# Optimization experiments

Hardware: AMD Instinct MI355X
Metric: run time of the kernel (lower is better)

## Reference

```python
import jax, jax.numpy as jnp
import numpy as np

M_DIM = 128   # vec_dim m
L_BAS = 64    # bas_dim L
RANK = 8      # sliding window length
BATCH = 32
SEQ = 2048


def _make_bbasis(L, m):
    # Bbasis[k, i] = cos(2*pi*(k+1)/(i+2)), fixed buffer
    k = jnp.arange(L, dtype=jnp.float32)[:, None]
    i = jnp.arange(m, dtype=jnp.float32)[None, :]
    return jnp.cos(2.0 * jnp.pi * (k + 1.0) / (i + 2.0))


def setup_inputs() -> dict:
    key = jax.random.key(0)
    k1, k2 = jax.random.split(key)
    seq_batch = jax.random.normal(k1, (BATCH, SEQ, M_DIM), dtype=jnp.float32)
    M = jnp.eye(M_DIM, dtype=jnp.float32)                     # nn.init.eye_
    Acoeff = jax.random.uniform(k2, (M_DIM, L_BAS), dtype=jnp.float32,
                                minval=-0.1, maxval=0.1)      # uniform(-0.1, 0.1)
    Bbasis = _make_bbasis(L_BAS, M_DIM)
    return {"seq_batch": seq_batch, "M": M, "Acoeff": Acoeff, "Bbasis": Bbasis}


def reference(seq_batch, M, Acoeff, Bbasis):
    B, S, m = seq_batch.shape
    L = Acoeff.shape[1]
    Nw = S - RANK + 1  # number of sliding windows (linear mode, stride 1)

    # unfold-equivalent: gather contiguous windows [B, Nw, RANK, m]
    idx = jnp.arange(Nw)[:, None] + jnp.arange(RANK)[None, :]
    windows = seq_batch[:, idx, :]
    agg = windows.mean(axis=2)              # rank_op='avg' -> [B, Nw, m]
    agg = jnp.einsum('bwm,nm->bwn', agg, M)  # agg @ M.T (linear map)

    # position-indexed basis target: N(k)[i] = Acoeff[i, k%L] * Bbasis[k%L, i]
    kmod = jnp.arange(Nw) % L
    Nk = Acoeff.T[kmod] * Bbasis[kmod]       # [Nw, m]

    # mean squared deviation over all windows / dims
    D = jnp.mean((agg - Nk[None, :, :]) ** 2)
    return D
```

## Files before the change

kernel.cpp:

```cpp
#include <hip/hip_runtime.h>

#define BATCH   32
#define SEQ     2048
#define MDIM    128
#define LBAS    64
#define NW      2041
#define WTILE   32
#define NROWS   40
#define APAD    136

typedef __attribute__((ext_vector_type(8))) short  short8;
typedef __attribute__((ext_vector_type(4))) float  float4v;

__device__ __forceinline__ unsigned short f2bf(float f) {
    unsigned int u = __float_as_uint(f);
    return (unsigned short)((u + 0x7FFFu + ((u >> 16) & 1u)) >> 16);
}

__global__ __launch_bounds__(256)
void ndd_prep(const float* __restrict__ Mmat,
              const float* __restrict__ Acoeff,
              const float* __restrict__ Bbasis,
              unsigned short* __restrict__ Mb,
              float* __restrict__ nk)
{
    const int gid = blockIdx.x * 256 + threadIdx.x;
    if (gid < 2048) {
        const int n = gid >> 4;
        const int c = gid & 15;
        const float* src = Mmat + n * MDIM + c * 8;
        short8 v;
        #pragma unroll
        for (int j = 0; j < 8; ++j) v[j] = (short)f2bf(src[j]);
        *reinterpret_cast<short8*>(Mb + ((size_t)(c * MDIM + n)) * 8) = v;
    } else if (gid < 2048 + 8192) {
        const int e = gid - 2048;
        const int k = e >> 7;
        const int n = e & 127;
        nk[k * MDIM + n] = Acoeff[n * LBAS + k] * Bbasis[k * MDIM + n];
    }
}

__global__ __launch_bounds__(256, 5)
void ndd_main(const float* __restrict__ x,
              const unsigned short* __restrict__ Mb,
              const float* __restrict__ nk,
              float* __restrict__ partial)
{
    __shared__ __align__(16) float sRaw[NROWS * MDIM];
    __shared__ __align__(16) unsigned short sA[WTILE * APAD];
    __shared__ float sred[4];

    const int tid  = threadIdx.x;
    const int lane = tid & 63;
    const int wave = tid >> 6;
    const int W0   = blockIdx.x * WTILE;
    const int b    = blockIdx.y;

    {
        const float* xb = x + ((size_t)b * SEQ + W0) * MDIM;
        #pragma unroll
        for (int i = 0; i < 5; ++i) {
            const int c = wave * 5 + i;
            if (W0 + 2 * c + 1 < SEQ) {
                const float* g = xb + c * 256 + lane * 4;
                __builtin_amdgcn_global_load_lds(
                    (const __attribute__((address_space(1))) void*)g,
                    (__attribute__((address_space(3))) void*)&sRaw[c * 256],
                    16, 0, 0);
            }
        }
    }
    __syncthreads();

    {
        const int m4 = tid & 31;
        const int w0 = (tid >> 5) * 4;
        const float4v* R = reinterpret_cast<const float4v*>(sRaw);
        float4v acc = {0.f, 0.f, 0.f, 0.f};
        #pragma unroll
        for (int r = 0; r < 8; ++r) acc += R[(w0 + r) * 32 + m4];
        #pragma unroll
        for (int j = 0; j < 4; ++j) {
            if (j) acc += R[(w0 + j + 7) * 32 + m4] - R[(w0 + j - 1) * 32 + m4];
            unsigned int lo = (unsigned)f2bf(acc.x * 0.125f) | ((unsigned)f2bf(acc.y * 0.125f) << 16);
            unsigned int hi = (unsigned)f2bf(acc.z * 0.125f) | ((unsigned)f2bf(acc.w * 0.125f) << 16);
            *reinterpret_cast<unsigned long long*>(&sA[(w0 + j) * APAD + m4 * 4]) =
                ((unsigned long long)hi << 32) | lo;
        }
    }
    __syncthreads();

    const int l15 = lane & 15;
    const int q   = lane >> 4;
    const int nb  = wave * 32;

    float4v accf[2][2];
    #pragma unroll
    for (int wi = 0; wi < 2; ++wi)
        #pragma unroll
        for (int nj = 0; nj < 2; ++nj)
            accf[wi][nj] = (float4v){0.f, 0.f, 0.f, 0.f};

    #pragma unroll
    for (int kk = 0; kk < 4; ++kk) {
        const int koff = kk * 32 + q * 8;
        short8 af[2], bfr[2];
        #pragma unroll
        for (int wi = 0; wi < 2; ++wi)
            af[wi] = *reinterpret_cast<const short8*>(&sA[(wi * 16 + l15) * APAD + koff]);
        #pragma unroll
        for (int nj = 0; nj < 2; ++nj)
            bfr[nj] = *reinterpret_cast<const short8*>(
                Mb + ((size_t)((kk * 4 + q) * MDIM + nb + nj * 16 + l15)) * 8);
        #pragma unroll
        for (int wi = 0; wi < 2; ++wi)
            #pragma unroll
            for (int nj = 0; nj < 2; ++nj)
                accf[wi][nj] = __builtin_amdgcn_mfma_f32_16x16x32_bf16(
                    af[wi], bfr[nj], accf[wi][nj], 0, 0, 0);
    }

    float local = 0.f;
    #pragma unroll
    for (int wi = 0; wi < 2; ++wi) {
        #pragma unroll
        for (int nj = 0; nj < 2; ++nj) {
            const int n = nb + nj * 16 + l15;
            #pragma unroll
            for (int r = 0; r < 4; ++r) {
                const int w = wi * 16 + q * 4 + r;
                if (W0 + w < NW) {
                    const float v = nk[((W0 + w) & 63) * MDIM + n];
                    const float d = accf[wi][nj][r] - v;
                    local += d * d;
                }
            }
        }
    }
    #pragma unroll
    for (int off = 32; off > 0; off >>= 1)
        local += __shfl_down(local, off, 64);
    if (lane == 0) sred[wave] = local;
    __syncthreads();
    if (tid == 0)
        partial[blockIdx.y * 64 + blockIdx.x] =
            (sred[0] + sred[1]) + (sred[2] + sred[3]);
}

__global__ __launch_bounds__(256)
void ndd_reduce(const float* __restrict__ partial, float* __restrict__ out)
{
    __shared__ float sred[4];
    float s = 0.f;
    #pragma unroll
    for (int i = 0; i < 8; ++i) s += partial[i * 256 + threadIdx.x];
    #pragma unroll
    for (int off = 32; off > 0; off >>= 1) s += __shfl_down(s, off, 64);
    if ((threadIdx.x & 63) == 0) sred[threadIdx.x >> 6] = s;
    __syncthreads();
    if (threadIdx.x == 0)
        out[0] = ((sred[0] + sred[1]) + (sred[2] + sred[3])) * (1.0f / 8359936.0f);
}

extern "C" void kernel_launch(void* const* d_in, const int* in_sizes, int n_in,
                              void* d_out, int out_size, void* d_ws, size_t ws_size,
                              hipStream_t stream) {
    const float* x     = (const float*)d_in[0];
    const float* Mmat  = (const float*)d_in[1];
    const float* Acoef = (const float*)d_in[2];
    const float* Bbas  = (const float*)d_in[3];
    float* out         = (float*)d_out;

    unsigned short* Mb = (unsigned short*)d_ws;
    float* nkp         = (float*)((char*)d_ws + 32768);
    float* part        = (float*)((char*)d_ws + 65536);

    ndd_prep<<<40, 256, 0, stream>>>(Mmat, Acoef, Bbas, Mb, nkp);
    dim3 grid(64, BATCH);
    ndd_main<<<grid, 256, 0, stream>>>(x, Mb, nkp, part);
    ndd_reduce<<<1, 256, 0, stream>>>(part, out);
}
```

Before: 89.53 us.

## Make main kernel persistent over four window tiles with double-buffered async loads

Each block now walks four consecutive 32-window tiles of one batch instead of one, so the grid drops from 2048 to 512 blocks. The raw input for the next tile is prefetched into a second LDS buffer via global_load_lds while the current tile's MFMA runs. The nk target rows are loaded into registers once per block, which works because tile starts are multiples of 32 and the pattern repeats every 64 windows. The cost is more LDS per block, lower occupancy (launch bounds 3), fewer blocks to spread across CUs, and a serial dependence across the four tiles.

New measurement: 85.70 us. 1.04x faster.

```diff
diff --git a/kernel.cpp b/kernel.cpp
--- a/kernel.cpp
+++ b/kernel.cpp
@@ -7,6 +7,7 @@
 #define NW      2041
 #define WTILE   32
 #define NROWS   40
+#define NT      4
 #define APAD    136
 
 typedef __attribute__((ext_vector_type(8))) short  short8;
@@ -41,120 +42,152 @@
     }
 }
 
-__global__ __launch_bounds__(256, 5)
+__global__ __launch_bounds__(256, 3)
 void ndd_main(const float* __restrict__ x,
               const unsigned short* __restrict__ Mb,
               const float* __restrict__ nk,
               float* __restrict__ partial)
 {
-    __shared__ __align__(16) float sRaw[NROWS * MDIM];
+    __shared__ __align__(16) float sRaw[2][NROWS * MDIM];
     __shared__ __align__(16) unsigned short sA[WTILE * APAD];
     __shared__ float sred[4];
 
     const int tid  = threadIdx.x;
     const int lane = tid & 63;
     const int wave = tid >> 6;
-    const int W0   = blockIdx.x * WTILE;
-    const int b    = blockIdx.y;
+    const int b    = blockIdx.x >> 4;
+    const int wtg  = blockIdx.x & 15;
+    const int l15  = lane & 15;
+    const int q    = lane >> 4;
+    const int nb   = wave * 32;
+
+    const float* xb = x + (size_t)b * SEQ * MDIM;
 
     {
-        const float* xb = x + ((size_t)b * SEQ + W0) * MDIM;
+        const int W0 = (wtg * NT) * WTILE;
         #pragma unroll
         for (int i = 0; i < 5; ++i) {
             const int c = wave * 5 + i;
-            if (W0 + 2 * c + 1 < SEQ) {
-                const float* g = xb + c * 256 + lane * 4;
+            if (2 * c + 1 <= 2047 - W0) {
+                const float* g = xb + (size_t)(W0 + 2 * c) * MDIM + lane * 4;
                 __builtin_amdgcn_global_load_lds(
                     (const __attribute__((address_space(1))) void*)g,
-                    (__attribute__((address_space(3))) void*)&sRaw[c * 256],
+                    (__attribute__((address_space(3))) void*)&sRaw[0][c * 256],
                     16, 0, 0);
             }
         }
     }
-    __syncthreads();
-
-    {
-        const int m4 = tid & 31;
-        const int w0 = (tid >> 5) * 4;
-        const float4v* R = reinterpret_cast<const float4v*>(sRaw);
-        float4v acc = {0.f, 0.f, 0.f, 0.f};
-        #pragma unroll
-        for (int r = 0; r < 8; ++r) acc += R[(w0 + r) * 32 + m4];
-        #pragma unroll
-        for (int j = 0; j < 4; ++j) {
-            if (j) acc += R[(w0 + j + 7) * 32 + m4] - R[(w0 + j - 1) * 32 + m4];
-            unsigned int lo = (unsigned)f2bf(acc.x * 0.125f) | ((unsigned)f2bf(acc.y * 0.125f) << 16);
-            unsigned int hi = (unsigned)f2bf(acc.z * 0.125f) | ((unsigned)f2bf(acc.w * 0.125f) << 16);
-            *reinterpret_cast<unsigned long long*>(&sA[(w0 + j) * APAD + m4 * 4]) =
-                ((unsigned long long)hi << 32) | lo;
+
+    float nkreg[2][2][2][4];
+    #pragma unroll
+    for (int p = 0; p < 2; ++p)
+        #pragma unroll
+        for (int wi = 0; wi < 2; ++wi)
+            #pragma unroll
+            for (int nj = 0; nj < 2; ++nj)
+                #pragma unroll
+                for (int r = 0; r < 4; ++r)
+                    nkreg[p][wi][nj][r] =
+                        nk[(p * 32 + wi * 16 + q * 4 + r) * MDIM + nb + nj * 16 + l15];
+
+    float local = 0.f;
+
+    for (int j = 0; j < NT; ++j) {
+        const int W0 = (wtg * NT + j) * WTILE;
+        const float4v* R = reinterpret_cast<const float4v*>(&sRaw[j & 1][0]);
+
+        __syncthreads();
+
+        {
+            const int m4 = tid & 31;
+            const int w0 = (tid >> 5) * 4;
+            float4v acc = {0.f, 0.f, 0.f, 0.f};
+            #pragma unroll
+            for (int r = 0; r < 8; ++r) acc += R[(w0 + r) * 32 + m4];
+            #pragma unroll
+            for (int t = 0; t < 4; ++t) {
+                if (t) acc += R[(w0 + t + 7) * 32 + m4] - R[(w0 + t - 1) * 32 + m4];
+                unsigned int lo = (unsigned)f2bf(acc.x * 0.125f) | ((unsigned)f2bf(acc.y * 0.125f) << 16);
+                unsigned int hi = (unsigned)f2bf(acc.z * 0.125f) | ((unsigned)f2bf(acc.w * 0.125f) << 16);
+                *reinterpret_cast<unsigned long long*>(&sA[(w0 + t) * APAD + m4 * 4]) =
+                    ((unsigned long long)hi << 32) | lo;
+            }
+        }
+
+        __syncthreads();
+
+        if (j + 1 < NT) {
+            const int W1 = (wtg * NT + j + 1) * WTILE;
+            #pragma unroll
+            for (int i = 0; i < 5; ++i) {
+                const int c = wave * 5 + i;
+                if (2 * c + 1 <= 2047 - W1) {
+                    const float* g = xb + (size_t)(W1 + 2 * c) * MDIM + lane * 4;
+                    __builtin_amdgcn_global_load_lds(
+                        (const __attribute__((address_space(1))) void*)g,
+                        (__attribute__((address_space(3))) void*)&sRaw[(j + 1) & 1][c * 256],
+                        16, 0, 0);
+                }
+            }
+        }
+
+        float4v accf[2][2];
+        #pragma unroll
+        for (int wi = 0; wi < 2; ++wi)
+            #pragma unroll
+            for (int nj = 0; nj < 2; ++nj)
+                accf[wi][nj] = (float4v){0.f, 0.f, 0.f, 0.f};
+
+        #pragma unroll
+        for (int kk = 0; kk < 4; ++kk) {
+            const int koff = kk * 32 + q * 8;
+            short8 af[2], bfr[2];
+            #pragma unroll
+            for (int wi = 0; wi < 2; ++wi)
+                af[wi] = *reinterpret_cast<const short8*>(&sA[(wi * 16 + l15) * APAD + koff]);
+            #pragma unroll
+            for (int nj = 0; nj < 2; ++nj)
+                bfr[nj] = *reinterpret_cast<const short8*>(
+                    Mb + ((size_t)((kk * 4 + q) * MDIM + nb + nj * 16 + l15)) * 8);
+            #pragma unroll
+            for (int wi = 0; wi < 2; ++wi)
+                #pragma unroll
+                for (int nj = 0; nj < 2; ++nj)
+                    accf[wi][nj] = __builtin_amdgcn_mfma_f32_16x16x32_bf16(
+                        af[wi], bfr[nj], accf[wi][nj], 0, 0, 0);
+        }
+
+        const int p = j & 1;
+        #pragma unroll
+        for (int wi = 0; wi < 2; ++wi) {
+            #pragma unroll
+            for (int nj = 0; nj < 2; ++nj) {
+                #pragma unroll
+                for (int r = 0; r < 4; ++r) {
+                    const int w = wi * 16 + q * 4 + r;
+                    if (W0 + w < NW) {
+                        const float d = accf[wi][nj][r] - nkreg[p][wi][nj][r];
+                        local += d * d;
+                    }
+                }
+            }
         }
     }
-    __syncthreads();
-
-    const int l15 = lane & 15;
-    const int q   = lane >> 4;
-    const int nb  = wave * 32;
-
-    float4v accf[2][2];
-    #pragma unroll
-    for (int wi = 0; wi < 2; ++wi)
-        #pragma unroll
-        for (int nj = 0; nj < 2; ++nj)
-            accf[wi][nj] = (float4v){0.f, 0.f, 0.f, 0.f};
-
-    #pragma unroll
-    for (int kk = 0; kk < 4; ++kk) {
-        const int koff = kk * 32 + q * 8;
-        short8 af[2], bfr[2];
-        #pragma unroll
-        for (int wi = 0; wi < 2; ++wi)
-            af[wi] = *reinterpret_cast<const short8*>(&sA[(wi * 16 + l15) * APAD + koff]);
-        #pragma unroll
-        for (int nj = 0; nj < 2; ++nj)
-            bfr[nj] = *reinterpret_cast<const short8*>(
-                Mb + ((size_t)((kk * 4 + q) * MDIM + nb + nj * 16 + l15)) * 8);
-        #pragma unroll
-        for (int wi = 0; wi < 2; ++wi)
-            #pragma unroll
-            for (int nj = 0; nj < 2; ++nj)
-                accf[wi][nj] = __builtin_amdgcn_mfma_f32_16x16x32_bf16(
-                    af[wi], bfr[nj], accf[wi][nj], 0, 0, 0);
-    }
-
-    float local = 0.f;
-    #pragma unroll
-    for (int wi = 0; wi < 2; ++wi) {
-        #pragma unroll
-        for (int nj = 0; nj < 2; ++nj) {
-            const int n = nb + nj * 16 + l15;
-            #pragma unroll
-            for (int r = 0; r < 4; ++r) {
-                const int w = wi * 16 + q * 4 + r;
-                if (W0 + w < NW) {
-                    const float v = nk[((W0 + w) & 63) * MDIM + n];
-                    const float d = accf[wi][nj][r] - v;
-                    local += d * d;
-                }
-            }
-        }
-    }
+
     #pragma unroll
     for (int off = 32; off > 0; off >>= 1)
         local += __shfl_down(local, off, 64);
     if (lane == 0) sred[wave] = local;
     __syncthreads();
     if (tid == 0)
-        partial[blockIdx.y * 64 + blockIdx.x] =
-            (sred[0] + sred[1]) + (sred[2] + sred[3]);
+        partial[blockIdx.x] = (sred[0] + sred[1]) + (sred[2] + sred[3]);
 }
 
 __global__ __launch_bounds__(256)
 void ndd_reduce(const float* __restrict__ partial, float* __restrict__ out)
 {
     __shared__ float sred[4];
-    float s = 0.f;
-    #pragma unroll
-    for (int i = 0; i < 8; ++i) s += partial[i * 256 + threadIdx.x];
+    float s = partial[threadIdx.x] + partial[threadIdx.x + 256];
     #pragma unroll
     for (int off = 32; off > 0; off >>= 1) s += __shfl_down(s, off, 64);
     if ((threadIdx.x & 63) == 0) sred[threadIdx.x >> 6] = s;
@@ -177,7 +210,6 @@
     float* part        = (float*)((char*)d_ws + 65536);
 
     ndd_prep<<<40, 256, 0, stream>>>(Mmat, Acoef, Bbas, Mb, nkp);
-    dim3 grid(64, BATCH);
-    ndd_main<<<grid, 256, 0, stream>>>(x, Mb, nkp, part);
+    ndd_main<<<512, 256, 0, stream>>>(x, Mb, nkp, part);
     ndd_reduce<<<1, 256, 0, stream>>>(part, out);
 }
```
